# Optimization experiments

Hardware: AMD Instinct MI355X
Metric: run time of the kernel (lower is better)

The kernel has to match this reference:

```python
import jax, jax.numpy as jnp
import numpy as np
import math

D_MODEL = 512
NHEAD = 8
HEAD_DIM = D_MODEL // NHEAD
MAX_REL = 128
B, T, S = 4, 2048, 2048


def setup_inputs() -> dict:
    key = jax.random.key(0)
    ks = jax.random.split(key, 16)
    sc = 1.0 / math.sqrt(D_MODEL)
    inp = {
        "query": jax.random.normal(ks[0], (B, T, D_MODEL), jnp.float32),
        "key": jax.random.normal(ks[1], (B, S, D_MODEL), jnp.float32),
        "value": jax.random.normal(ks[2], (B, S, D_MODEL), jnp.float32),
        "Wq": jax.random.normal(ks[3], (D_MODEL, D_MODEL), jnp.float32) * sc,
        "bq": jnp.zeros((D_MODEL,), jnp.float32),
        "Wk": jax.random.normal(ks[4], (D_MODEL, D_MODEL), jnp.float32) * sc,
        "bk": jnp.zeros((D_MODEL,), jnp.float32),
        "Wv": jax.random.normal(ks[5], (D_MODEL, D_MODEL), jnp.float32) * sc,
        "bv": jnp.zeros((D_MODEL,), jnp.float32),
        "Wo": jax.random.normal(ks[6], (D_MODEL, D_MODEL), jnp.float32) * sc,
        "bo": jnp.zeros((D_MODEL,), jnp.float32),
        "rel_emb": jax.random.normal(ks[7], (2 * MAX_REL + 1, NHEAD), jnp.float32) * 0.02,
    }
    return inp


def reference(query, key, value, Wq, bq, Wk, bk, Wv, bv, Wo, bo, rel_emb):
    # linear projections (torch Linear: x @ W.T + b), split heads -> [B,H,T,Dh]
    def proj(x, W, b, L):
        return (x @ W.T + b).reshape(B, L, NHEAD, HEAD_DIM).transpose(0, 2, 1, 3)

    q = proj(query, Wq, bq, T)
    k = proj(key, Wk, bk, S)
    v = proj(value, Wv, bv, S)

    scores = jnp.einsum("bhtd,bhsd->bhts", q, k) / math.sqrt(HEAD_DIM)

    # relative position bias lookup: rel[t,s] = clamp(t-s) + max_rel -> [H,T,S]
    rel = jnp.arange(T)[:, None] - jnp.arange(S)[None, :]
    rel = jnp.clip(rel, -MAX_REL, MAX_REL) + MAX_REL
    bias = rel_emb[rel].transpose(2, 0, 1)  # [H,T,S]
    scores = scores + bias[None]

    w = jax.nn.softmax(scores, axis=-1)  # dropout p used in eval mode -> identity
    out = jnp.einsum("bhts,bhsd->bhtd", w, v)
    out = out.transpose(0, 2, 1, 3).reshape(B, T, D_MODEL)
    return out @ Wo.T + bo
```

## Files before the change

### kernel.cpp

```cpp
#include <hip/hip_runtime.h>

typedef __attribute__((ext_vector_type(4))) float f32x4;
typedef __attribute__((ext_vector_type(16))) float f32x16;
typedef __attribute__((ext_vector_type(4))) unsigned short u16x4;
typedef __attribute__((ext_vector_type(8))) unsigned short u16x8;
typedef __attribute__((ext_vector_type(4))) unsigned int u32x4;
typedef __attribute__((ext_vector_type(8))) __bf16 bf16x8;

#define SZX_E ((size_t)4 * 2048 * 512)
#define SZW_E ((size_t)512 * 512)

__device__ __forceinline__ unsigned short f2bf(float f) {
  unsigned int u = __builtin_bit_cast(unsigned int, f);
  u += 0x7fffu + ((u >> 16) & 1u);
  return (unsigned short)(u >> 16);
}

__device__ __forceinline__ bf16x8 ld_bf8(const unsigned short* p) {
  return __builtin_bit_cast(bf16x8, *(const u16x8*)p);
}

__device__ __forceinline__ f32x4 mfma16(bf16x8 a, bf16x8 b, f32x4 c) {
  return __builtin_amdgcn_mfma_f32_16x16x32_bf16(a, b, c, 0, 0, 0);
}

__device__ __forceinline__ f32x16 mfma32(bf16x8 a, bf16x8 b, f32x16 c) {
  return __builtin_amdgcn_mfma_f32_32x32x16_bf16(a, b, c, 0, 0, 0);
}

__device__ __forceinline__ unsigned int cvt_pk_bf16(float lo, float hi) {
  unsigned int r;
  asm("v_cvt_pk_bf16_f32 %0, %1, %2" : "=v"(r) : "v"(lo), "v"(hi));
  return r;
}

__device__ __forceinline__ void plane32_swap(unsigned int& a, unsigned int& b) {
  asm("v_permlane32_swap_b32 %0, %1" : "+v"(a), "+v"(b));
}

__device__ __forceinline__ float exp2_fast(float x) {
  float r;
  asm("v_exp_f32 %0, %1" : "=v"(r) : "v"(x));
  return r;
}

__device__ __forceinline__ void gload16(const void* g, void* l) {
  __builtin_amdgcn_global_load_lds(
      (const __attribute__((address_space(1))) unsigned int*)g,
      (__attribute__((address_space(3))) unsigned int*)l, 16, 0, 0);
}

__global__ __launch_bounds__(256) void cvt_all(const float* __restrict__ q_,
                                               const float* __restrict__ k_,
                                               const float* __restrict__ v_,
                                               const float* __restrict__ wq_,
                                               const float* __restrict__ wk_,
                                               const float* __restrict__ wv_,
                                               const float* __restrict__ wo_,
                                               unsigned short* __restrict__ out) {
  const int bq = blockIdx.x;
  const float* src;
  size_t segbase, li;
  if (bq < 12288) {
    const int s = bq >> 12;
    src = (s == 0) ? q_ : (s == 1) ? k_ : v_;
    li = (size_t)(bq & 4095) * 256 + threadIdx.x;
    segbase = (size_t)s * 4194304;
  } else {
    const int s = (bq - 12288) >> 8;
    src = (s == 0) ? wq_ : (s == 1) ? wk_ : (s == 2) ? wv_ : wo_;
    li = (size_t)((bq - 12288) & 255) * 256 + threadIdx.x;
    segbase = 12582912 + (size_t)s * 262144;
  }
  const f32x4 v = *(const f32x4*)(src + li * 4);
  u16x4 r;
  r[0] = f2bf(v[0]); r[1] = f2bf(v[1]); r[2] = f2bf(v[2]); r[3] = f2bf(v[3]);
  *(u16x4*)(out + segbase + li * 4) = r;
}

__global__ __launch_bounds__(256) void gemm_qkv(const unsigned short* __restrict__ base,
                                                const float* __restrict__ bq,
                                                const float* __restrict__ bk,
                                                const float* __restrict__ bv,
                                                unsigned short* __restrict__ outb) {
  __shared__ unsigned short Asb[2][4096];
  __shared__ unsigned short Bsb[2][4096];
  const int z = blockIdx.z;
  const unsigned short* A = base + (size_t)z * SZX_E;
  const unsigned short* Bw = base + 3 * SZX_E + (size_t)z * SZW_E;
  const float* bias = (z == 0) ? bq : (z == 1) ? bk : bv;

  const int tid = threadIdx.x;
  const int l = tid & 63;
  const int w = tid >> 6;
  const int g = l >> 4;
  const int lr = l & 15;
  const int mB = blockIdx.y * 128;
  const int nB = blockIdx.x * 128;
  const int m0 = (w >> 1) * 64;
  const int n0 = (w & 1) * 64;
  const int ubase = tid & ~63;

  auto stage = [&](int bufi, int kk) {
#pragma unroll
    for (int i = 0; i < 2; i++) {
      const int idx = i * 256 + tid;
      const int ub = i * 256 + ubase;
      const int r = idx >> 2, c = idx & 3;
      gload16((const char*)A + ((size_t)(mB + r) * 512 + kk + c * 8) * 2,
              (char*)&Asb[bufi][0] + ub * 16);
      gload16((const char*)Bw + ((size_t)(nB + r) * 512 + kk + c * 8) * 2,
              (char*)&Bsb[bufi][0] + ub * 16);
    }
  };

  f32x4 acc[4][4];
#pragma unroll
  for (int i = 0; i < 4; i++)
#pragma unroll
    for (int j = 0; j < 4; j++) acc[i][j] = f32x4{0.f, 0.f, 0.f, 0.f};

  stage(0, 0);
  __syncthreads();
  int buf = 0;

  for (int ks = 0; ks < 16; ++ks) {
    if (ks < 15) stage(buf ^ 1, (ks + 1) * 32);
    bf16x8 af[4], bfr[4];
#pragma unroll
    for (int t = 0; t < 4; t++) {
      af[t] = ld_bf8(&Asb[buf][(m0 + t * 16 + lr) * 32 + g * 8]);
      bfr[t] = ld_bf8(&Bsb[buf][(n0 + t * 16 + lr) * 32 + g * 8]);
    }
#pragma unroll
    for (int i = 0; i < 4; i++)
#pragma unroll
      for (int j = 0; j < 4; j++)
        acc[i][j] = mfma16(af[i], bfr[j], acc[i][j]);
    __syncthreads();
    buf ^= 1;
  }

  unsigned short* outz = outb + (size_t)z * SZX_E;
#pragma unroll
  for (int j = 0; j < 4; j++) {
    const int n = nB + n0 + j * 16 + lr;
    const float bn = bias[n];
#pragma unroll
    for (int i = 0; i < 4; i++) {
#pragma unroll
      for (int r = 0; r < 4; r++) {
        const int m = mB + m0 + i * 16 + g * 4 + r;
        const float v = acc[i][j][r] + bn;
        if (z < 2) {
          outz[(size_t)m * 512 + n] = f2bf(v);
        } else {
          const int bb = m >> 11, s = m & 2047;
          const int hh = n >> 6, d = n & 63;
          outz[((size_t)((bb * 8 + hh) * 64 + d) << 11) + s] = f2bf(v);
        }
      }
    }
  }
}

__global__ __launch_bounds__(256) void gemm_o(const unsigned short* __restrict__ A,
                                              const unsigned short* __restrict__ Bw,
                                              const float* __restrict__ bias,
                                              float* __restrict__ Cout) {
  __shared__ unsigned short Asb[2][4096];
  __shared__ unsigned short Bsb[2][4096];
  const int tid = threadIdx.x;
  const int l = tid & 63;
  const int w = tid >> 6;
  const int g = l >> 4;
  const int lr = l & 15;
  const int mB = blockIdx.y * 128;
  const int nB = blockIdx.x * 128;
  const int m0 = (w >> 1) * 64;
  const int n0 = (w & 1) * 64;
  const int ubase = tid & ~63;

  auto stage = [&](int bufi, int kk) {
#pragma unroll
    for (int i = 0; i < 2; i++) {
      const int idx = i * 256 + tid;
      const int ub = i * 256 + ubase;
      const int r = idx >> 2, c = idx & 3;
      gload16((const char*)A + ((size_t)(mB + r) * 512 + kk + c * 8) * 2,
              (char*)&Asb[bufi][0] + ub * 16);
      gload16((const char*)Bw + ((size_t)(nB + r) * 512 + kk + c * 8) * 2,
              (char*)&Bsb[bufi][0] + ub * 16);
    }
  };

  f32x4 acc[4][4];
#pragma unroll
  for (int i = 0; i < 4; i++)
#pragma unroll
    for (int j = 0; j < 4; j++) acc[i][j] = f32x4{0.f, 0.f, 0.f, 0.f};

  stage(0, 0);
  __syncthreads();
  int buf = 0;

  for (int ks = 0; ks < 16; ++ks) {
    if (ks < 15) stage(buf ^ 1, (ks + 1) * 32);
    bf16x8 af[4], bfr[4];
#pragma unroll
    for (int t = 0; t < 4; t++) {
      af[t] = ld_bf8(&Asb[buf][(m0 + t * 16 + lr) * 32 + g * 8]);
      bfr[t] = ld_bf8(&Bsb[buf][(n0 + t * 16 + lr) * 32 + g * 8]);
    }
#pragma unroll
    for (int i = 0; i < 4; i++)
#pragma unroll
      for (int j = 0; j < 4; j++)
        acc[i][j] = mfma16(af[i], bfr[j], acc[i][j]);
    __syncthreads();
    buf ^= 1;
  }

#pragma unroll
  for (int j = 0; j < 4; j++) {
    const int n = nB + n0 + j * 16 + lr;
    const float bn = bias[n];
#pragma unroll
    for (int i = 0; i < 4; i++) {
#pragma unroll
      for (int r = 0; r < 4; r++) {
        const int m = mB + m0 + i * 16 + g * 4 + r;
        Cout[(size_t)m * 512 + n] = acc[i][j][r] + bn;
      }
    }
  }
}

__global__ __launch_bounds__(256, 2) void attn_kernel(const unsigned short* __restrict__ Qp,
                                                      const unsigned short* __restrict__ Kp,
                                                      const unsigned short* __restrict__ Vt,
                                                      const float* __restrict__ rel_emb,
                                                      unsigned short* __restrict__ At) {
  __shared__ float bias_s[257];
  __shared__ unsigned short K_lds[2][4096];
  __shared__ unsigned short V_lds[2][4096];
  const int bid0 = blockIdx.x;
  const int lg = (bid0 & 7) * 64 + (bid0 >> 3);
  const int qb = lg & 15;
  const int h = (lg >> 4) & 7;
  const int b = lg >> 7;
  const int tid = threadIdx.x;
  const int lane = tid & 63, w = tid >> 6;
  const int hi = lane >> 5, q31 = lane & 31;
  const int q0w = qb * 128 + w * 32;
  const int tq = q0w + q31;
  const float SCL = 0.125f * 1.44269504f;

  const char* kstage = (const char*)Kp + ((size_t)b * 2048 * 512 + h * 64) * 2;
  const char* vstage = (const char*)Vt + ((size_t)(b * 8 + h) * 64 * 2048) * 2;

  auto stage = [&](int bufi, int s0n) {
#pragma unroll
    for (int ii = 0; ii < 4; ii++) {
      const int ins = (w & 1) * 4 + ii;
      const int rr = ins * 8 + (lane >> 3);
      const int ch = (lane & 7) ^ (rr & 7);
      if (w < 2) {
        gload16(kstage + (size_t)(s0n + rr) * 1024 + ch * 16,
                (char*)&K_lds[bufi][0] + ins * 1024);
      } else {
        gload16(vstage + (size_t)rr * 4096 + (size_t)s0n * 2 + ch * 16,
                (char*)&V_lds[bufi][0] + ins * 1024);
      }
    }
  };

  for (int i = tid; i < 257; i += 256) bias_s[i] = rel_emb[i * 8 + h] * 1.44269504f;
  stage(0, 0);
  __syncthreads();
  const float bias_lo = bias_s[0], bias_hi = bias_s[256];

  const unsigned short* qptr = Qp + (size_t)(b * 2048 + tq) * 512 + h * 64 + hi * 8;
  const bf16x8 qf0 = ld_bf8(qptr);
  const bf16x8 qf1 = ld_bf8(qptr + 16);
  const bf16x8 qf2 = ld_bf8(qptr + 32);
  const bf16x8 qf3 = ld_bf8(qptr + 48);

  const f32x16 z16 = {0.f, 0.f, 0.f, 0.f, 0.f, 0.f, 0.f, 0.f,
                      0.f, 0.f, 0.f, 0.f, 0.f, 0.f, 0.f, 0.f};
  f32x16 o_lo = z16, o_hi = z16;
  float m_run = -1e30f, l_run = 0.f;
  int buf = 0;

  for (int t = 0; t < 32; ++t) {
    const int s0 = t * 64;
    if (t != 31) stage(buf ^ 1, s0 + 64);

    const unsigned short* kb = &K_lds[buf][0];
    const int rswz = q31 & 7;
    f32x16 sa, sb;
    sa = mfma32(ld_bf8(kb + q31 * 64 + (((0 + hi) ^ rswz) << 3)), qf0, z16);
    sb = mfma32(ld_bf8(kb + (32 + q31) * 64 + (((0 + hi) ^ rswz) << 3)), qf0, z16);
    sa = mfma32(ld_bf8(kb + q31 * 64 + (((2 + hi) ^ rswz) << 3)), qf1, sa);
    sb = mfma32(ld_bf8(kb + (32 + q31) * 64 + (((2 + hi) ^ rswz) << 3)), qf1, sb);
    sa = mfma32(ld_bf8(kb + q31 * 64 + (((4 + hi) ^ rswz) << 3)), qf2, sa);
    sb = mfma32(ld_bf8(kb + (32 + q31) * 64 + (((4 + hi) ^ rswz) << 3)), qf2, sb);
    sa = mfma32(ld_bf8(kb + q31 * 64 + (((6 + hi) ^ rswz) << 3)), qf3, sa);
    sb = mfma32(ld_bf8(kb + (32 + q31) * 64 + (((6 + hi) ^ rswz) << 3)), qf3, sb);

    const unsigned short* vb = &V_lds[buf][0];
    bf16x8 vl[4], vh[4];
#pragma unroll
    for (int ks = 0; ks < 4; ks++) {
      vl[ks] = ld_bf8(vb + q31 * 64 + (((ks * 2 + hi) ^ rswz) << 3));
      vh[ks] = ld_bf8(vb + (32 + q31) * 64 + (((ks * 2 + hi) ^ rswz) << 3));
    }

    const int relmin = q0w - s0 - 63;
    const int relmax = q0w + 31 - s0;
    float SCL2, off0;
    if (relmin >= 128 || relmax <= -128) {
      SCL2 = SCL;
      off0 = (relmin >= 128) ? bias_hi : bias_lo;
    } else {
#pragma unroll
      for (int r = 0; r < 16; r++) {
        const int rowA = (r & 3) + 8 * (r >> 2) + 4 * hi;
        const int rA = tq - s0 - rowA;
        const int rB = rA - 32;
        const int iA = (rA < -128 ? -128 : (rA > 128 ? 128 : rA)) + 128;
        const int iB = (rB < -128 ? -128 : (rB > 128 ? 128 : rB)) + 128;
        sa[r] = fmaf(sa[r], SCL, bias_s[iA]);
        sb[r] = fmaf(sb[r], SCL, bias_s[iB]);
      }
      SCL2 = 1.f;
      off0 = 0.f;
    }

    const float t0 = fmaxf(fmaxf(sa[0], sa[1]), sa[2]);
    const float t1 = fmaxf(fmaxf(sa[3], sa[4]), sa[5]);
    const float t2 = fmaxf(fmaxf(sa[6], sa[7]), sa[8]);
    const float t3 = fmaxf(fmaxf(sa[9], sa[10]), sa[11]);
    const float t4 = fmaxf(fmaxf(sa[12], sa[13]), sa[14]);
    const float t5 = fmaxf(fmaxf(sa[15], sb[0]), sb[1]);
    const float t6 = fmaxf(fmaxf(sb[2], sb[3]), sb[4]);
    const float t7 = fmaxf(fmaxf(sb[5], sb[6]), sb[7]);
    const float t8 = fmaxf(fmaxf(sb[8], sb[9]), sb[10]);
    const float t9 = fmaxf(fmaxf(sb[11], sb[12]), sb[13]);
    const float ta = fmaxf(sb[14], sb[15]);
    const float u0 = fmaxf(fmaxf(t0, t1), t2);
    const float u1 = fmaxf(fmaxf(t3, t4), t5);
    const float u2 = fmaxf(fmaxf(t6, t7), t8);
    float mx = fmaxf(fmaxf(fmaxf(u0, u1), u2), fmaxf(t9, ta));
    mx = fmaf(mx, SCL2, off0);
    mx = fmaxf(mx, __shfl_xor(mx, 32, 64));

    if (!__all(mx <= m_run + 8.f)) {
      const float m_new = fmaxf(m_run, mx);
      const float rsq = exp2_fast(m_run - m_new);
      l_run *= rsq;
      m_run = m_new;
#pragma unroll
      for (int r2 = 0; r2 < 16; r2++) {
        const int ro = (r2 & 3) + 8 * (r2 >> 2) + 4 * hi;
        const float rr = __shfl(rsq, ro, 64);
        o_lo[r2] *= rr;
        o_hi[r2] *= rr;
      }
    }

    const float ea = off0 - m_run;
#pragma unroll
    for (int r = 0; r < 16; r++) {
      sa[r] = exp2_fast(fmaf(sa[r], SCL2, ea));
      sb[r] = exp2_fast(fmaf(sb[r], SCL2, ea));
    }
    float s8[8];
#pragma unroll
    for (int i = 0; i < 8; i++)
      s8[i] = (sa[i] + sa[i + 8]) + (sb[i] + sb[i + 8]);
    float ps = ((s8[0] + s8[1]) + (s8[2] + s8[3])) + ((s8[4] + s8[5]) + (s8[6] + s8[7]));
    ps += __shfl_xor(ps, 32, 64);
    l_run += ps;

    bf16x8 pa[4];
#pragma unroll
    for (int ks = 0; ks < 4; ks++) {
      const int c8 = (ks & 1) * 8;
      const f32x16& src = (ks < 2) ? sa : sb;
      unsigned int a0 = cvt_pk_bf16(src[c8 + 0], src[c8 + 1]);
      unsigned int b0 = cvt_pk_bf16(src[c8 + 4], src[c8 + 5]);
      unsigned int a1 = cvt_pk_bf16(src[c8 + 2], src[c8 + 3]);
      unsigned int b1 = cvt_pk_bf16(src[c8 + 6], src[c8 + 7]);
      plane32_swap(a0, b0);
      plane32_swap(a1, b1);
      pa[ks] = __builtin_bit_cast(bf16x8, u32x4{a0, a1, b0, b1});
    }

#pragma unroll
    for (int ks = 0; ks < 4; ks++) {
      o_lo = mfma32(pa[ks], vl[ks], o_lo);
      o_hi = mfma32(pa[ks], vh[ks], o_hi);
    }

    __syncthreads();
    buf ^= 1;
  }

  const float inv = 1.f / l_run;
#pragma unroll
  for (int r2 = 0; r2 < 16; r2++) {
    const int ro = (r2 & 3) + 8 * (r2 >> 2) + 4 * hi;
    const float rr = __shfl(inv, ro, 64);
    unsigned short* op = At + (size_t)(b * 2048 + q0w + ro) * 512 + h * 64;
    op[q31] = f2bf(o_lo[r2] * rr);
    op[32 + q31] = f2bf(o_hi[r2] * rr);
  }
}

extern "C" void kernel_launch(void* const* d_in, const int* in_sizes, int n_in,
                              void* d_out, int out_size, void* d_ws, size_t ws_size,
                              hipStream_t stream) {
  const float* query = (const float*)d_in[0];
  const float* key   = (const float*)d_in[1];
  const float* value = (const float*)d_in[2];
  const float* Wq = (const float*)d_in[3];
  const float* bq = (const float*)d_in[4];
  const float* Wk = (const float*)d_in[5];
  const float* bk = (const float*)d_in[6];
  const float* Wv = (const float*)d_in[7];
  const float* bv = (const float*)d_in[8];
  const float* Wo = (const float*)d_in[9];
  const float* bo = (const float*)d_in[10];
  const float* rel = (const float*)d_in[11];

  char* ws = (char*)d_ws;
  unsigned short* base = (unsigned short*)ws;
  unsigned short* wo = base + 3 * SZX_E + 3 * SZW_E;
  unsigned short* Qp = base + 3 * SZX_E + 4 * SZW_E;
  unsigned short* Kp = Qp + SZX_E;
  unsigned short* Vt = Kp + SZX_E;
  unsigned short* At = Vt + SZX_E;

  cvt_all<<<dim3(13312), dim3(256), 0, stream>>>(query, key, value, Wq, Wk, Wv, Wo, base);

  dim3 blk(256);
  gemm_qkv<<<dim3(4, 64, 3), blk, 0, stream>>>(base, bq, bk, bv, Qp);

  attn_kernel<<<dim3(512), blk, 0, stream>>>(Qp, Kp, Vt, rel, At);

  gemm_o<<<dim3(4, 64), blk, 0, stream>>>(At, wo, bo, (float*)d_out);
}
```

Before: 110.2 us.

## Fuse fp32-to-bf16 activation cast into QKV GEMM; widen attention KV tile

```diff
diff --git a/kernel.cpp b/kernel.cpp
--- a/kernel.cpp
+++ b/kernel.cpp
@@ -50,44 +50,34 @@
       (__attribute__((address_space(3))) unsigned int*)l, 16, 0, 0);
 }
 
-__global__ __launch_bounds__(256) void cvt_all(const float* __restrict__ q_,
-                                               const float* __restrict__ k_,
-                                               const float* __restrict__ v_,
-                                               const float* __restrict__ wq_,
-                                               const float* __restrict__ wk_,
-                                               const float* __restrict__ wv_,
-                                               const float* __restrict__ wo_,
-                                               unsigned short* __restrict__ out) {
+__global__ __launch_bounds__(256) void cvt_w(const float* __restrict__ wq_,
+                                             const float* __restrict__ wk_,
+                                             const float* __restrict__ wv_,
+                                             const float* __restrict__ wo_,
+                                             unsigned short* __restrict__ out) {
   const int bq = blockIdx.x;
-  const float* src;
-  size_t segbase, li;
-  if (bq < 12288) {
-    const int s = bq >> 12;
-    src = (s == 0) ? q_ : (s == 1) ? k_ : v_;
-    li = (size_t)(bq & 4095) * 256 + threadIdx.x;
-    segbase = (size_t)s * 4194304;
-  } else {
-    const int s = (bq - 12288) >> 8;
-    src = (s == 0) ? wq_ : (s == 1) ? wk_ : (s == 2) ? wv_ : wo_;
-    li = (size_t)((bq - 12288) & 255) * 256 + threadIdx.x;
-    segbase = 12582912 + (size_t)s * 262144;
-  }
+  const int s = bq >> 8;
+  const float* src = (s == 0) ? wq_ : (s == 1) ? wk_ : (s == 2) ? wv_ : wo_;
+  const size_t li = (size_t)(bq & 255) * 256 + threadIdx.x;
   const f32x4 v = *(const f32x4*)(src + li * 4);
   u16x4 r;
   r[0] = f2bf(v[0]); r[1] = f2bf(v[1]); r[2] = f2bf(v[2]); r[3] = f2bf(v[3]);
-  *(u16x4*)(out + segbase + li * 4) = r;
-}
-
-__global__ __launch_bounds__(256) void gemm_qkv(const unsigned short* __restrict__ base,
+  *(u16x4*)(out + (size_t)s * SZW_E + li * 4) = r;
+}
+
+__global__ __launch_bounds__(256) void gemm_qkv(const float* __restrict__ q_,
+                                                const float* __restrict__ k_,
+                                                const float* __restrict__ v_,
+                                                const unsigned short* __restrict__ wbase,
                                                 const float* __restrict__ bq,
                                                 const float* __restrict__ bk,
                                                 const float* __restrict__ bv,
                                                 unsigned short* __restrict__ outb) {
-  __shared__ unsigned short Asb[2][4096];
+  __shared__ float Asb[2][4096];
   __shared__ unsigned short Bsb[2][4096];
   const int z = blockIdx.z;
-  const unsigned short* A = base + (size_t)z * SZX_E;
-  const unsigned short* Bw = base + 3 * SZX_E + (size_t)z * SZW_E;
+  const float* A = (z == 0) ? q_ : (z == 1) ? k_ : v_;
+  const unsigned short* Bw = wbase + (size_t)z * SZW_E;
   const float* bias = (z == 0) ? bq : (z == 1) ? bk : bv;
 
   const int tid = threadIdx.x;
@@ -103,12 +93,19 @@
 
   auto stage = [&](int bufi, int kk) {
 #pragma unroll
+    for (int i = 0; i < 4; i++) {
+      const int idx = i * 256 + tid;
+      const int ub = i * 256 + ubase;
+      const int r = idx >> 3, c4 = idx & 7;
+      const int col = ((((c4 >> 1) ^ (r & 3)) << 1) | (c4 & 1)) << 2;
+      gload16((const char*)A + ((size_t)(mB + r) * 512 + kk + col) * 4,
+              (char*)&Asb[bufi][0] + ub * 16);
+    }
+#pragma unroll
     for (int i = 0; i < 2; i++) {
       const int idx = i * 256 + tid;
       const int ub = i * 256 + ubase;
       const int r = idx >> 2, c = idx & 3;
-      gload16((const char*)A + ((size_t)(mB + r) * 512 + kk + c * 8) * 2,
-              (char*)&Asb[bufi][0] + ub * 16);
       gload16((const char*)Bw + ((size_t)(nB + r) * 512 + kk + c * 8) * 2,
               (char*)&Bsb[bufi][0] + ub * 16);
     }
@@ -129,7 +126,16 @@
     bf16x8 af[4], bfr[4];
 #pragma unroll
     for (int t = 0; t < 4; t++) {
-      af[t] = ld_bf8(&Asb[buf][(m0 + t * 16 + lr) * 32 + g * 8]);
+      const int ar = m0 + t * 16 + lr;
+      const float* arow = &Asb[buf][ar * 32 + ((g ^ (ar & 3)) << 3)];
+      const f32x4 a0 = *(const f32x4*)arow;
+      const f32x4 a1 = *(const f32x4*)(arow + 4);
+      u32x4 ap;
+      ap[0] = cvt_pk_bf16(a0[0], a0[1]);
+      ap[1] = cvt_pk_bf16(a0[2], a0[3]);
+      ap[2] = cvt_pk_bf16(a1[0], a1[1]);
+      ap[3] = cvt_pk_bf16(a1[2], a1[3]);
+      af[t] = __builtin_bit_cast(bf16x8, ap);
       bfr[t] = ld_bf8(&Bsb[buf][(n0 + t * 16 + lr) * 32 + g * 8]);
     }
 #pragma unroll
@@ -242,8 +248,8 @@
                                                       const float* __restrict__ rel_emb,
                                                       unsigned short* __restrict__ At) {
   __shared__ float bias_s[257];
-  __shared__ unsigned short K_lds[2][4096];
-  __shared__ unsigned short V_lds[2][4096];
+  __shared__ unsigned short K_lds[2][8192];
+  __shared__ unsigned short V_lds[2][8192];
   const int bid0 = blockIdx.x;
   const int lg = (bid0 & 7) * 64 + (bid0 >> 3);
   const int qb = lg & 15;
@@ -261,15 +267,17 @@
 
   auto stage = [&](int bufi, int s0n) {
 #pragma unroll
-    for (int ii = 0; ii < 4; ii++) {
-      const int ins = (w & 1) * 4 + ii;
-      const int rr = ins * 8 + (lane >> 3);
-      const int ch = (lane & 7) ^ (rr & 7);
+    for (int ii = 0; ii < 8; ii++) {
+      const int ins = (w & 1) * 8 + ii;
       if (w < 2) {
+        const int rr = ins * 8 + (lane >> 3);
+        const int ch = (lane & 7) ^ (rr & 7);
         gload16(kstage + (size_t)(s0n + rr) * 1024 + ch * 16,
                 (char*)&K_lds[bufi][0] + ins * 1024);
       } else {
-        gload16(vstage + (size_t)rr * 4096 + (size_t)s0n * 2 + ch * 16,
+        const int d = ins * 4 + (lane >> 4);
+        const int scn = (lane & 15) ^ (d & 7);
+        gload16(vstage + (size_t)d * 4096 + (size_t)s0n * 2 + scn * 16,
                 (char*)&V_lds[bufi][0] + ins * 1024);
       }
     }
@@ -292,31 +300,31 @@
   float m_run = -1e30f, l_run = 0.f;
   int buf = 0;
 
-  for (int t = 0; t < 32; ++t) {
-    const int s0 = t * 64;
-    if (t != 31) stage(buf ^ 1, s0 + 64);
+  for (int t = 0; t < 16; ++t) {
+    const int s0 = t * 128;
+    if (t != 15) stage(buf ^ 1, s0 + 128);
 
     const unsigned short* kb = &K_lds[buf][0];
     const int rswz = q31 & 7;
-    f32x16 sa, sb;
-    sa = mfma32(ld_bf8(kb + q31 * 64 + (((0 + hi) ^ rswz) << 3)), qf0, z16);
-    sb = mfma32(ld_bf8(kb + (32 + q31) * 64 + (((0 + hi) ^ rswz) << 3)), qf0, z16);
-    sa = mfma32(ld_bf8(kb + q31 * 64 + (((2 + hi) ^ rswz) << 3)), qf1, sa);
-    sb = mfma32(ld_bf8(kb + (32 + q31) * 64 + (((2 + hi) ^ rswz) << 3)), qf1, sb);
-    sa = mfma32(ld_bf8(kb + q31 * 64 + (((4 + hi) ^ rswz) << 3)), qf2, sa);
-    sb = mfma32(ld_bf8(kb + (32 + q31) * 64 + (((4 + hi) ^ rswz) << 3)), qf2, sb);
-    sa = mfma32(ld_bf8(kb + q31 * 64 + (((6 + hi) ^ rswz) << 3)), qf3, sa);
-    sb = mfma32(ld_bf8(kb + (32 + q31) * 64 + (((6 + hi) ^ rswz) << 3)), qf3, sb);
-
-    const unsigned short* vb = &V_lds[buf][0];
-    bf16x8 vl[4], vh[4];
-#pragma unroll
-    for (int ks = 0; ks < 4; ks++) {
-      vl[ks] = ld_bf8(vb + q31 * 64 + (((ks * 2 + hi) ^ rswz) << 3));
-      vh[ks] = ld_bf8(vb + (32 + q31) * 64 + (((ks * 2 + hi) ^ rswz) << 3));
-    }
-
-    const int relmin = q0w - s0 - 63;
+    f32x16 sa, sb, sc, sd;
+    sa = mfma32(ld_bf8(kb + (q31)*64       + (((0 + hi) ^ rswz) << 3)), qf0, z16);
+    sb = mfma32(ld_bf8(kb + (32 + q31)*64  + (((0 + hi) ^ rswz) << 3)), qf0, z16);
+    sc = mfma32(ld_bf8(kb + (64 + q31)*64  + (((0 + hi) ^ rswz) << 3)), qf0, z16);
+    sd = mfma32(ld_bf8(kb + (96 + q31)*64  + (((0 + hi) ^ rswz) << 3)), qf0, z16);
+    sa = mfma32(ld_bf8(kb + (q31)*64       + (((2 + hi) ^ rswz) << 3)), qf1, sa);
+    sb = mfma32(ld_bf8(kb + (32 + q31)*64  + (((2 + hi) ^ rswz) << 3)), qf1, sb);
+    sc = mfma32(ld_bf8(kb + (64 + q31)*64  + (((2 + hi) ^ rswz) << 3)), qf1, sc);
+    sd = mfma32(ld_bf8(kb + (96 + q31)*64  + (((2 + hi) ^ rswz) << 3)), qf1, sd);
+    sa = mfma32(ld_bf8(kb + (q31)*64       + (((4 + hi) ^ rswz) << 3)), qf2, sa);
+    sb = mfma32(ld_bf8(kb + (32 + q31)*64  + (((4 + hi) ^ rswz) << 3)), qf2, sb);
+    sc = mfma32(ld_bf8(kb + (64 + q31)*64  + (((4 + hi) ^ rswz) << 3)), qf2, sc);
+    sd = mfma32(ld_bf8(kb + (96 + q31)*64  + (((4 + hi) ^ rswz) << 3)), qf2, sd);
+    sa = mfma32(ld_bf8(kb + (q31)*64       + (((6 + hi) ^ rswz) << 3)), qf3, sa);
+    sb = mfma32(ld_bf8(kb + (32 + q31)*64  + (((6 + hi) ^ rswz) << 3)), qf3, sb);
+    sc = mfma32(ld_bf8(kb + (64 + q31)*64  + (((6 + hi) ^ rswz) << 3)), qf3, sc);
+    sd = mfma32(ld_bf8(kb + (96 + q31)*64  + (((6 + hi) ^ rswz) << 3)), qf3, sd);
+
+    const int relmin = q0w - s0 - 127;
     const int relmax = q0w + 31 - s0;
     float SCL2, off0;
     if (relmin >= 128 || relmax <= -128) {
@@ -328,30 +336,30 @@
         const int rowA = (r & 3) + 8 * (r >> 2) + 4 * hi;
         const int rA = tq - s0 - rowA;
         const int rB = rA - 32;
+        const int rC = rA - 64;
+        const int rD = rA - 96;
         const int iA = (rA < -128 ? -128 : (rA > 128 ? 128 : rA)) + 128;
         const int iB = (rB < -128 ? -128 : (rB > 128 ? 128 : rB)) + 128;
+        const int iC = (rC < -128 ? -128 : (rC > 128 ? 128 : rC)) + 128;
+        const int iD = (rD < -128 ? -128 : (rD > 128 ? 128 : rD)) + 128;
         sa[r] = fmaf(sa[r], SCL, bias_s[iA]);
         sb[r] = fmaf(sb[r], SCL, bias_s[iB]);
+        sc[r] = fmaf(sc[r], SCL, bias_s[iC]);
+        sd[r] = fmaf(sd[r], SCL, bias_s[iD]);
       }
       SCL2 = 1.f;
       off0 = 0.f;
     }
 
-    const float t0 = fmaxf(fmaxf(sa[0], sa[1]), sa[2]);
-    const float t1 = fmaxf(fmaxf(sa[3], sa[4]), sa[5]);
-    const float t2 = fmaxf(fmaxf(sa[6], sa[7]), sa[8]);
-    const float t3 = fmaxf(fmaxf(sa[9], sa[10]), sa[11]);
-    const float t4 = fmaxf(fmaxf(sa[12], sa[13]), sa[14]);
-    const float t5 = fmaxf(fmaxf(sa[15], sb[0]), sb[1]);
-    const float t6 = fmaxf(fmaxf(sb[2], sb[3]), sb[4]);
-    const float t7 = fmaxf(fmaxf(sb[5], sb[6]), sb[7]);
-    const float t8 = fmaxf(fmaxf(sb[8], sb[9]), sb[10]);
-    const float t9 = fmaxf(fmaxf(sb[11], sb[12]), sb[13]);
-    const float ta = fmaxf(sb[14], sb[15]);
-    const float u0 = fmaxf(fmaxf(t0, t1), t2);
-    const float u1 = fmaxf(fmaxf(t3, t4), t5);
-    const float u2 = fmaxf(fmaxf(t6, t7), t8);
-    float mx = fmaxf(fmaxf(fmaxf(u0, u1), u2), fmaxf(t9, ta));
+    float m01[16];
+#pragma unroll
+    for (int r = 0; r < 16; r++)
+      m01[r] = fmaxf(fmaxf(sa[r], sb[r]), fmaxf(sc[r], sd[r]));
+    float p0 = fmaxf(fmaxf(m01[0], m01[1]), fmaxf(m01[2], m01[3]));
+    float p1 = fmaxf(fmaxf(m01[4], m01[5]), fmaxf(m01[6], m01[7]));
+    float p2 = fmaxf(fmaxf(m01[8], m01[9]), fmaxf(m01[10], m01[11]));
+    float p3 = fmaxf(fmaxf(m01[12], m01[13]), fmaxf(m01[14], m01[15]));
+    float mx = fmaxf(fmaxf(p0, p1), fmaxf(p2, p3));
     mx = fmaf(mx, SCL2, off0);
     mx = fmaxf(mx, __shfl_xor(mx, 32, 64));
 
@@ -374,33 +382,67 @@
     for (int r = 0; r < 16; r++) {
       sa[r] = exp2_fast(fmaf(sa[r], SCL2, ea));
       sb[r] = exp2_fast(fmaf(sb[r], SCL2, ea));
-    }
-    float s8[8];
-#pragma unroll
-    for (int i = 0; i < 8; i++)
-      s8[i] = (sa[i] + sa[i + 8]) + (sb[i] + sb[i + 8]);
-    float ps = ((s8[0] + s8[1]) + (s8[2] + s8[3])) + ((s8[4] + s8[5]) + (s8[6] + s8[7]));
+      sc[r] = exp2_fast(fmaf(sc[r], SCL2, ea));
+      sd[r] = exp2_fast(fmaf(sd[r], SCL2, ea));
+    }
+    float s01[16];
+#pragma unroll
+    for (int r = 0; r < 16; r++)
+      s01[r] = (sa[r] + sb[r]) + (sc[r] + sd[r]);
+    float q0s = (s01[0] + s01[1]) + (s01[2] + s01[3]);
+    float q1s = (s01[4] + s01[5]) + (s01[6] + s01[7]);
+    float q2s = (s01[8] + s01[9]) + (s01[10] + s01[11]);
+    float q3s = (s01[12] + s01[13]) + (s01[14] + s01[15]);
+    float ps = (q0s + q1s) + (q2s + q3s);
     ps += __shfl_xor(ps, 32, 64);
     l_run += ps;
 
-    bf16x8 pa[4];
-#pragma unroll
-    for (int ks = 0; ks < 4; ks++) {
-      const int c8 = (ks & 1) * 8;
-      const f32x16& src = (ks < 2) ? sa : sb;
-      unsigned int a0 = cvt_pk_bf16(src[c8 + 0], src[c8 + 1]);
-      unsigned int b0 = cvt_pk_bf16(src[c8 + 4], src[c8 + 5]);
-      unsigned int a1 = cvt_pk_bf16(src[c8 + 2], src[c8 + 3]);
-      unsigned int b1 = cvt_pk_bf16(src[c8 + 6], src[c8 + 7]);
-      plane32_swap(a0, b0);
-      plane32_swap(a1, b1);
-      pa[ks] = __builtin_bit_cast(bf16x8, u32x4{a0, a1, b0, b1});
-    }
-
-#pragma unroll
-    for (int ks = 0; ks < 4; ks++) {
-      o_lo = mfma32(pa[ks], vl[ks], o_lo);
-      o_hi = mfma32(pa[ks], vh[ks], o_hi);
+    const unsigned short* vb = &V_lds[buf][0];
+    {
+      bf16x8 pa[4];
+#pragma unroll
+      for (int ks = 0; ks < 4; ks++) {
+        const int c8 = (ks & 1) * 8;
+        const f32x16& src = (ks < 2) ? sa : sb;
+        unsigned int a0 = cvt_pk_bf16(src[c8 + 0], src[c8 + 1]);
+        unsigned int b0 = cvt_pk_bf16(src[c8 + 4], src[c8 + 5]);
+        unsigned int a1 = cvt_pk_bf16(src[c8 + 2], src[c8 + 3]);
+        unsigned int b1 = cvt_pk_bf16(src[c8 + 6], src[c8 + 7]);
+        plane32_swap(a0, b0);
+        plane32_swap(a1, b1);
+        pa[ks] = __builtin_bit_cast(bf16x8, u32x4{a0, a1, b0, b1});
+      }
+#pragma unroll
+      for (int ks = 0; ks < 4; ks++) {
+        const int j = ks * 2 + hi;
+        const bf16x8 vl = ld_bf8(vb + q31 * 128 + ((j ^ rswz) << 3));
+        const bf16x8 vh = ld_bf8(vb + (32 + q31) * 128 + ((j ^ rswz) << 3));
+        o_lo = mfma32(pa[ks], vl, o_lo);
+        o_hi = mfma32(pa[ks], vh, o_hi);
+      }
+    }
+    {
+      bf16x8 pa[4];
+#pragma unroll
+      for (int ks = 0; ks < 4; ks++) {
+        const int c8 = (ks & 1) * 8;
+        const f32x16& src = (ks < 2) ? sc : sd;
+        unsigned int a0 = cvt_pk_bf16(src[c8 + 0], src[c8 + 1]);
+        unsigned int b0 = cvt_pk_bf16(src[c8 + 4], src[c8 + 5]);
+        unsigned int a1 = cvt_pk_bf16(src[c8 + 2], src[c8 + 3]);
+        unsigned int b1 = cvt_pk_bf16(src[c8 + 6], src[c8 + 7]);
+        plane32_swap(a0, b0);
+        plane32_swap(a1, b1);
+        pa[ks] = __builtin_bit_cast(bf16x8, u32x4{a0, a1, b0, b1});
+      }
+#pragma unroll
+      for (int ks = 0; ks < 4; ks++) {
+        const int j = (ks + 4) * 2 + hi;
+        const bf16x8 vl = ld_bf8(vb + q31 * 128 + ((j ^ rswz) << 3));
+        const bf16x8 vh = ld_bf8(vb + (32 + q31) * 128 + ((j ^ rswz) << 3));
+        o_lo = mfma32(pa[ks], vl, o_lo);
+        o_hi = mfma32(pa[ks], vh, o_hi);
+      }
     }
 
     __syncthreads();
@@ -435,19 +477,18 @@
   const float* rel = (const float*)d_in[11];
 
   char* ws = (char*)d_ws;
-  unsigned short* base = (unsigned short*)ws;
-  unsigned short* wo = base + 3 * SZX_E + 3 * SZW_E;
-  unsigned short* Qp = base + 3 * SZX_E + 4 * SZW_E;
+  unsigned short* wgt = (unsigned short*)ws;
+  unsigned short* Qp = wgt + 4 * SZW_E;
   unsigned short* Kp = Qp + SZX_E;
   unsigned short* Vt = Kp + SZX_E;
   unsigned short* At = Vt + SZX_E;
 
-  cvt_all<<<dim3(13312), dim3(256), 0, stream>>>(query, key, value, Wq, Wk, Wv, Wo, base);
-
   dim3 blk(256);
-  gemm_qkv<<<dim3(4, 64, 3), blk, 0, stream>>>(base, bq, bk, bv, Qp);
+  cvt_w<<<dim3(1024), blk, 0, stream>>>(Wq, Wk, Wv, Wo, wgt);
+
+  gemm_qkv<<<dim3(4, 64, 3), blk, 0, stream>>>(query, key, value, wgt, bq, bk, bv, Qp);
 
   attn_kernel<<<dim3(512), blk, 0, stream>>>(Qp, Kp, Vt, rel, At);
 
-  gemm_o<<<dim3(4, 64), blk, 0, stream>>>(At, wo, bo, (float*)d_out);
-}
+  gemm_o<<<dim3(4, 64), blk, 0, stream>>>(At, wgt + 3 * SZW_E, bo, (float*)d_out);
+}
```

Result: slower. 115.3 us (+4.6%).
